# Kernel optimization log

Measured on AMD Instinct MI355X. Metric: run time of the kernel, lower is better.

## Reference

```python
import jax, jax.numpy as jnp
import numpy as np

B, S, T = 64, 128, 32
H, E, VOC = 512, 512, 32000
A = 2 * H  # atten_size


def setup_inputs() -> dict:
    key = jax.random.key(0)
    ks = jax.random.split(key, 10)
    n = lambda k, shp, sc: jax.random.normal(k, shp, jnp.float32) * sc
    return dict(
        encoder_output=n(ks[0], (B, S, A), 1.0),
        hs0=n(ks[1], (B, H), 1.0),
        cs0=n(ks[2], (B, H), 1.0),
        target=n(ks[3], (B, T, E), 1.0),
        wh_w=n(ks[4], (A, A), 0.02),          # Conv2d(2H, 2H, 1, bias=False) weight [out,in]
        ws_w=n(ks[5], (A, A), 0.02),          # Linear(2H, 2H)
        ws_b=jnp.zeros((A,), jnp.float32),
        we_w=n(ks[6], (A,), 0.02),            # Conv1d(2H, 1, 1, bias=False) weight [in]
        W_ih=n(ks[7], (4 * H, E), 0.02),      # LSTMCell params (torch gate order i,f,g,o)
        W_hh=n(ks[8], (4 * H, H), 0.02),
        b_ih=jnp.zeros((4 * H,), jnp.float32),
        b_hh=jnp.zeros((4 * H,), jnp.float32),
        Vp_w=n(ks[9], (VOC, 3 * H), 0.02),    # Linear(H + 2H, vocab)
        Vp_b=jnp.zeros((VOC,), jnp.float32),
    )


def reference(encoder_output, hs0, cs0, target, wh_w, ws_w, ws_b, we_w,
              W_ih, W_hh, b_ih, b_hh, Vp_w, Vp_b):
    # Faithful to torch: .view() is a raw row-major reshape, NOT a transpose.
    eo = encoder_output.reshape(B, A, S)                 # view(B, 2H, 1, S), squeeze the 1
    conv = jnp.einsum('oc,bcs->bos', wh_w, eo)           # 1x1 conv2d over channels
    enc_feat = conv.reshape(B, S, A)                     # view(B, -1, atten_size)

    def step(carry, x_t):
        hs, cs = carry
        df = jnp.concatenate([hs, cs], axis=1) @ ws_w.T + ws_b        # [B, A]
        comb = (enc_feat + df[:, None, :]).reshape(B, A, S)           # view(B, 2H, -1)
        e = jnp.einsum('c,bcs->bs', we_w, jnp.tanh(comb))             # conv1d(2H->1), squeeze
        a = jax.nn.softmax(e, axis=1)                                 # [B, S]
        h_star = jnp.einsum('bs,bsh->bh', a, encoder_output)          # bmm, squeeze
        # LSTMCell (torch gate order: i, f, g, o)
        gates = x_t @ W_ih.T + b_ih + hs @ W_hh.T + b_hh
        i, f, g, o = jnp.split(gates, 4, axis=1)
        cs_n = jax.nn.sigmoid(f) * cs + jax.nn.sigmoid(i) * jnp.tanh(g)
        hs_n = jax.nn.sigmoid(o) * jnp.tanh(cs_n)
        feat = jnp.concatenate([h_star, hs_n], axis=1)                # [B, 3H]
        out = jax.nn.log_softmax(feat @ Vp_w.T + Vp_b, axis=1)        # [B, vocab]
        return (hs_n, cs_n), out

    _, outs = jax.lax.scan(step, (hs0, cs0), jnp.swapaxes(target, 0, 1))
    return outs  # [T, B, vocab] (torch returns a list of T [B, vocab] arrays)
```

## Files before the change

### kernel.cpp

```cpp
#include <hip/hip_runtime.h>
#include <hip/hip_bf16.h>
#include <cstdint>
#include <cstddef>

typedef unsigned short u16;
typedef __attribute__((ext_vector_type(8))) short s16x8;
typedef __attribute__((ext_vector_type(4))) float f32x4;
typedef __attribute__((ext_vector_type(4))) unsigned short u16x4;

__device__ __forceinline__ float b2f(u16 u){ unsigned int i = ((unsigned int)u)<<16; float f; __builtin_memcpy(&f,&i,4); return f; }
__device__ __forceinline__ u16 f2b(float f){ unsigned int i; __builtin_memcpy(&i,&f,4); i = (i + 0x7fffu + ((i>>16)&1u))>>16; return (u16)i; }
__device__ __forceinline__ float tanh_f(float x){ return 1.f - 2.f/(1.f + __expf(2.f*x)); }
__device__ __forceinline__ float sig_f(float x){ return 1.f/(1.f + __expf(-x)); }

__device__ __forceinline__ void cp16(const u16* g, u16* l) {
  __builtin_amdgcn_global_load_lds((const __attribute__((address_space(1))) unsigned int*)g,
                                   (__attribute__((address_space(3))) unsigned int*)l, 16, 0, 0);
}

__global__ void k_cvt(const float* __restrict__ src, u16* __restrict__ dst, int n4) {
  int i = blockIdx.x*256 + threadIdx.x;
  if (i >= n4) return;
  float4 v = ((const float4*)src)[i];
  u16x4 o; o.x = f2b(v.x); o.y = f2b(v.y); o.z = f2b(v.z); o.w = f2b(v.w);
  ((u16x4*)dst)[i] = o;
}

__global__ __launch_bounds__(256, 2) void gemm_bt(
    const u16* __restrict__ A, const u16* __restrict__ B, void* __restrict__ Cv,
    const float* __restrict__ bias1, const float* __restrict__ bias2,
    int M, int N, int K, int ldA, int ldB, int ldC,
    long long strideA, long long strideB, long long strideC, int outBf16, int swz)
{
  __shared__ u16 As[128*32];
  __shared__ u16 Bs[128*32];
  const int bz = blockIdx.z;
  const u16* Ab = A + (size_t)bz*strideA;
  const u16* Bb = B + (size_t)bz*strideB;
  int bxx = blockIdx.x, byy = blockIdx.y;
  if (swz) {
    int nx = gridDim.x, ny = gridDim.y;
    int nwg = nx * ny;
    int orig = byy * nx + bxx;
    int cpx = nwg >> 3;
    int id = (orig & 7) * cpx + (orig >> 3);
    byy = id % ny;
    bxx = id / ny;
  }
  const int tn = bxx * 128;
  const int tm = byy * 128;
  const int tid = threadIdx.x, wid = tid>>6, lane = tid&63;
  const int wm = wid & 1, wn = wid >> 1;
  const int lrow = lane & 15, lk = (lane>>4)*8;

  f32x4 acc[4][4];
  #pragma unroll
  for (int i=0;i<4;++i)
    #pragma unroll
    for (int j=0;j<4;++j) acc[i][j] = (f32x4){0.f,0.f,0.f,0.f};

  const int srow = lane>>2;
  const int scol = (lane&3)*8;

  for (int k0 = 0; k0 < K; k0 += 32) {
    int c0 = wid, c1 = wid + 4;
    cp16(Ab + (size_t)(tm + c0*16 + srow)*ldA + k0 + scol, As + c0*512);
    cp16(Ab + (size_t)(tm + c1*16 + srow)*ldA + k0 + scol, As + c1*512);
    cp16(Bb + (size_t)(tn + c0*16 + srow)*ldB + k0 + scol, Bs + c0*512);
    cp16(Bb + (size_t)(tn + c1*16 + srow)*ldB + k0 + scol, Bs + c1*512);
    __syncthreads();

    s16x8 af[4], bfr[4];
    #pragma unroll
    for (int mt=0; mt<4; ++mt)
      af[mt] = *(const s16x8*)(As + (size_t)(wm*64 + mt*16 + lrow)*32 + lk);
    #pragma unroll
    for (int nt=0; nt<4; ++nt)
      bfr[nt] = *(const s16x8*)(Bs + (size_t)(wn*64 + nt*16 + lrow)*32 + lk);
    #pragma unroll
    for (int mt=0; mt<4; ++mt)
      #pragma unroll
      for (int nt=0; nt<4; ++nt)
        acc[mt][nt] = __builtin_amdgcn_mfma_f32_16x16x32_bf16(af[mt], bfr[nt], acc[mt][nt], 0,0,0);
    __syncthreads();
  }

  float* Cf = (float*)Cv + (size_t)bz*strideC;
  u16*   Ch = (u16*)Cv + (size_t)bz*strideC;
  #pragma unroll
  for (int mt=0; mt<4; ++mt) {
    #pragma unroll
    for (int nt=0; nt<4; ++nt) {
      int col = tn + wn*64 + nt*16 + (lane&15);
      float badd = 0.f;
      if (bias1) badd += bias1[col];
      if (bias2) badd += bias2[col];
      #pragma unroll
      for (int r=0; r<4; ++r) {
        int row = tm + wm*64 + mt*16 + (lane>>4)*4 + r;
        float v = acc[mt][nt][r] + badd;
        if (outBf16) Ch[(size_t)row*ldC + col] = f2b(v);
        else         Cf[(size_t)row*ldC + col] = v;
      }
    }
  }
}

__global__ __launch_bounds__(256, 2) void gemm_a16b32(
    const u16* __restrict__ A, const float* __restrict__ B, float* __restrict__ C,
    const float* __restrict__ bias, int M, int N, int K, int ldA, int ldB, int ldC, int swz)
{
  __shared__ u16 As[128*32];
  __shared__ u16 Bs[128*32];
  int bxx = blockIdx.x, byy = blockIdx.y;
  if (swz) {
    int nx = gridDim.x, ny = gridDim.y;
    int nwg = nx * ny;
    int orig = byy * nx + bxx;
    int cpx = nwg >> 3;
    int id = (orig & 7) * cpx + (orig >> 3);
    byy = id % ny;
    bxx = id / ny;
  }
  const int tn = bxx * 128;
  const int tm = byy * 128;
  const int tid = threadIdx.x, wid = tid>>6, lane = tid&63;
  const int wm = wid & 1, wn = wid >> 1;
  const int lrow = lane & 15, lk = (lane>>4)*8;

  f32x4 acc[4][4];
  #pragma unroll
  for (int i=0;i<4;++i)
    #pragma unroll
    for (int j=0;j<4;++j) acc[i][j] = (f32x4){0.f,0.f,0.f,0.f};

  const int srow = lane>>2;
  const int scol = (lane&3)*8;
  const int brow0 = tid>>3;
  const int bcol  = (tid&7)*4;

  for (int k0 = 0; k0 < K; k0 += 32) {
    int c0 = wid, c1 = wid + 4;
    cp16(A + (size_t)(tm + c0*16 + srow)*ldA + k0 + scol, As + c0*512);
    cp16(A + (size_t)(tm + c1*16 + srow)*ldA + k0 + scol, As + c1*512);
    #pragma unroll
    for (int rr=0; rr<4; ++rr) {
      int row = rr*32 + brow0;
      float4 v = *(const float4*)(B + (size_t)(tn + row)*ldB + k0 + bcol);
      u16x4 o; o.x = f2b(v.x); o.y = f2b(v.y); o.z = f2b(v.z); o.w = f2b(v.w);
      *(u16x4*)(Bs + (size_t)row*32 + bcol) = o;
    }
    __syncthreads();

    s16x8 af[4], bfr[4];
    #pragma unroll
    for (int mt=0; mt<4; ++mt)
      af[mt] = *(const s16x8*)(As + (size_t)(wm*64 + mt*16 + lrow)*32 + lk);
    #pragma unroll
    for (int nt=0; nt<4; ++nt)
      bfr[nt] = *(const s16x8*)(Bs + (size_t)(wn*64 + nt*16 + lrow)*32 + lk);
    #pragma unroll
    for (int mt=0; mt<4; ++mt)
      #pragma unroll
      for (int nt=0; nt<4; ++nt)
        acc[mt][nt] = __builtin_amdgcn_mfma_f32_16x16x32_bf16(af[mt], bfr[nt], acc[mt][nt], 0,0,0);
    __syncthreads();
  }

  #pragma unroll
  for (int mt=0; mt<4; ++mt) {
    #pragma unroll
    for (int nt=0; nt<4; ++nt) {
      int col = tn + wn*64 + nt*16 + (lane&15);
      float badd = bias ? bias[col] : 0.f;
      #pragma unroll
      for (int r=0; r<4; ++r) {
        int row = tm + wm*64 + mt*16 + (lane>>4)*4 + r;
        C[(size_t)row*ldC + col] = acc[mt][nt][r] + badd;
      }
    }
  }
}

__global__ void k_init(const float* __restrict__ hs0, const float* __restrict__ cs0,
                       u16* __restrict__ HSb0, u16* __restrict__ CSb0, float* __restrict__ CS0) {
  int i = blockIdx.x*256 + threadIdx.x;
  HSb0[i] = f2b(hs0[i]);
  float c = cs0[i];
  CSb0[i] = f2b(c);
  CS0[i] = c;
}

__global__ void k_x2(const float* __restrict__ target, u16* __restrict__ X2) {
  int r = blockIdx.x;
  int t = r >> 6, b = r & 63;
  float4 v = ((const float4*)(target + ((size_t)b*32 + t)*512))[threadIdx.x];
  u16x4 o; o.x = f2b(v.x); o.y = f2b(v.y); o.z = f2b(v.z); o.w = f2b(v.w);
  *(u16x4*)(X2 + (size_t)r*512 + threadIdx.x*4) = o;
}

__global__ void k_ebt(const float* __restrict__ enc, u16* __restrict__ EBt) {
  __shared__ u16 tile[64][72];
  int b = blockIdx.z;
  int c0 = blockIdx.x*64, s0 = blockIdx.y*64;
  int tid = threadIdx.x;
  int j = tid & 63, i0 = tid >> 6;
  const float* src = enc + (size_t)b*131072;
  for (int i = i0; i < 64; i += 4)
    tile[i][j] = f2b(src[(size_t)(c0+i)*128 + (s0+j)]);
  __syncthreads();
  u16* dst = EBt + (size_t)b*131072;
  for (int i = i0; i < 64; i += 4)
    dst[(size_t)(s0+i)*1024 + (c0+j)] = tile[j][i];
}

__global__ __launch_bounds__(256, 1) void lstm_step(
    const u16* __restrict__ HSb_t, const float* __restrict__ CS_t,
    const u16* __restrict__ Whh, const float* __restrict__ Xg_t,
    u16* __restrict__ HSb_n, float* __restrict__ CS_n, u16* __restrict__ CSb_n)
{
  int tid = threadIdx.x, wid = tid>>6, lane = tid&63;
  int hc = blockIdx.x * 16;
  int lr = lane & 15, lk = (lane>>4)*8;
  f32x4 acc[4];
  #pragma unroll
  for (int q=0;q<4;++q) acc[q] = (f32x4){0.f,0.f,0.f,0.f};
  int brow = wid*16 + lr;
  #pragma unroll
  for (int k0 = 0; k0 < 512; k0 += 32) {
    s16x8 a = *(const s16x8*)(HSb_t + (size_t)brow*512 + k0 + lk);
    #pragma unroll
    for (int q=0;q<4;++q) {
      int gj = q*512 + hc + lr;
      s16x8 bb = *(const s16x8*)(Whh + (size_t)gj*512 + k0 + lk);
      acc[q] = __builtin_amdgcn_mfma_f32_16x16x32_bf16(a, bb, acc[q], 0,0,0);
    }
  }
  int h = hc + lr;
  #pragma unroll
  for (int r=0;r<4;++r) {
    int b = wid*16 + (lane>>4)*4 + r;
    float gi = acc[0][r] + Xg_t[(size_t)b*2048 + h];
    float gf = acc[1][r] + Xg_t[(size_t)b*2048 + 512 + h];
    float gg = acc[2][r] + Xg_t[(size_t)b*2048 + 1024 + h];
    float go = acc[3][r] + Xg_t[(size_t)b*2048 + 1536 + h];
    float cs = CS_t[(size_t)b*512 + h];
    float csn = sig_f(gf)*cs + sig_f(gi)*tanh_f(gg);
    float hsn = sig_f(go)*tanh_f(csn);
    CS_n[(size_t)b*512 + h] = csn;
    HSb_n[(size_t)b*512 + h] = f2b(hsn);
    CSb_n[(size_t)b*512 + h] = f2b(csn);
  }
}

__global__ void k_dfa(const u16* __restrict__ HSb, const u16* __restrict__ CSb, u16* __restrict__ DfA) {
  int r = blockIdx.x; int t = r >> 6, b = r & 63;
  const uint2* hs = (const uint2*)(HSb + ((size_t)t*64 + b)*512);
  const uint2* cs = (const uint2*)(CSb + ((size_t)t*64 + b)*512);
  uint2* dst = (uint2*)(DfA + (size_t)r*1024);
  int tid = threadIdx.x;
  dst[tid] = (tid < 128) ? hs[tid] : cs[tid-128];
}

__global__ __launch_bounds__(256) void k_attn(
    const u16* __restrict__ G, const float* __restrict__ df,
    const float* __restrict__ we_w, const u16* __restrict__ Enc16,
    const u16* __restrict__ HSb, u16* __restrict__ Feat)
{
  int r = blockIdx.x, t = r>>6, b = r&63;
  int tid = threadIdx.x;
  __shared__ float weS[1024];
  __shared__ float eP[2][128];
  __shared__ float aS[128];
  __shared__ float redM, redS;
  for (int i=tid;i<1024;i+=256) weS[i] = we_w[i];
  __syncthreads();
  int s = tid & 127, cg = tid >> 7;
  const u16* Gb = G + (size_t)b*131072;
  const float* dfr = df + (size_t)r*1024;
  float p = 0.f;
  #pragma unroll 8
  for (int c = cg*512; c < cg*512 + 512; ++c) {
    float x = b2f(Gb[(size_t)c*128 + s]) + dfr[((c&7)<<7) + s];
    p += weS[c]*tanh_f(x);
  }
  eP[cg][s] = p;
  __syncthreads();
  if (tid < 128) aS[tid] = eP[0][tid] + eP[1][tid];
  __syncthreads();
  if (tid < 64) {
    float m = fmaxf(aS[tid], aS[tid+64]);
    #pragma unroll
    for (int off=32; off; off>>=1) m = fmaxf(m, __shfl_xor(m, off, 64));
    float sm = __expf(aS[tid]-m) + __expf(aS[tid+64]-m);
    #pragma unroll
    for (int off=32; off; off>>=1) sm += __shfl_xor(sm, off, 64);
    if (tid==0){ redM = m; redS = sm; }
  }
  __syncthreads();
  if (tid < 128) aS[tid] = __expf(aS[tid]-redM)/redS;
  __syncthreads();
  const u16* encb = Enc16 + (size_t)b*131072;
  u16* Fr = Feat + (size_t)r*1536;
  int h4 = tid*4;
  float a0=0,a1=0,a2=0,a3=0;
  for (int s2=0;s2<128;++s2) {
    float av = aS[s2];
    u16x4 v = *(const u16x4*)(encb + (size_t)s2*1024 + h4);
    a0 += av*b2f(v.x); a1 += av*b2f(v.y); a2 += av*b2f(v.z); a3 += av*b2f(v.w);
  }
  u16x4 o; o.x = f2b(a0); o.y = f2b(a1); o.z = f2b(a2); o.w = f2b(a3);
  *(u16x4*)(Fr + h4) = o;
  const u16* hsn = HSb + ((size_t)(t+1)*64 + b)*512;
  if (tid < 128) *(u16x4*)(Fr + 1024 + tid*4) = *(const u16x4*)(hsn + tid*4);
}

__global__ __launch_bounds__(256) void k_lsm(float* __restrict__ out) {
  int r = blockIdx.x;
  float* row = out + (size_t)r*32000;
  int tid = threadIdx.x, wid = tid>>6;
  __shared__ float redA[4], redB[4];
  float m = -3.0e38f;
  for (int i = tid*4; i < 32000; i += 1024) {
    float4 v = *(const float4*)(row + i);
    m = fmaxf(m, fmaxf(fmaxf(v.x, v.y), fmaxf(v.z, v.w)));
  }
  #pragma unroll
  for (int off=32; off; off>>=1) m = fmaxf(m, __shfl_xor(m, off, 64));
  if ((tid&63)==0) redA[wid] = m;
  __syncthreads();
  m = fmaxf(fmaxf(redA[0],redA[1]), fmaxf(redA[2],redA[3]));
  float sacc = 0.f;
  for (int i = tid*4; i < 32000; i += 1024) {
    float4 v = *(const float4*)(row + i);
    sacc += __expf(v.x-m) + __expf(v.y-m) + __expf(v.z-m) + __expf(v.w-m);
  }
  #pragma unroll
  for (int off=32; off; off>>=1) sacc += __shfl_xor(sacc, off, 64);
  if ((tid&63)==0) redB[wid] = sacc;
  __syncthreads();
  float lse = m + logf(redB[0]+redB[1]+redB[2]+redB[3]);
  for (int i = tid*4; i < 32000; i += 1024) {
    float4 v = *(const float4*)(row + i);
    v.x -= lse; v.y -= lse; v.z -= lse; v.w -= lse;
    *(float4*)(row + i) = v;
  }
}

extern "C" void kernel_launch(void* const* d_in, const int* in_sizes, int n_in,
                              void* d_out, int out_size, void* d_ws, size_t ws_size,
                              hipStream_t stream) {
  (void)in_sizes; (void)n_in; (void)out_size;
  const float* enc    = (const float*)d_in[0];
  const float* hs0    = (const float*)d_in[1];
  const float* cs0    = (const float*)d_in[2];
  const float* target = (const float*)d_in[3];
  const float* wh_w   = (const float*)d_in[4];
  const float* ws_w   = (const float*)d_in[5];
  const float* ws_b   = (const float*)d_in[6];
  const float* we_w   = (const float*)d_in[7];
  const float* W_ih   = (const float*)d_in[8];
  const float* W_hh   = (const float*)d_in[9];
  const float* b_ih   = (const float*)d_in[10];
  const float* b_hh   = (const float*)d_in[11];
  const float* Vp_w   = (const float*)d_in[12];
  const float* Vp_b   = (const float*)d_in[13];
  float* out = (float*)d_out;

  char* ws = (char*)d_ws;
  u16*   X2    = (u16*)  (ws + 0);
  u16*   EBt   = (u16*)  (ws + 2097152);
  u16*   G     = (u16*)  (ws + 18874368);
  float* Xg    = (float*)(ws + 35651584);
  u16*   Enc16 = (u16*)  (ws + 35651584);
  u16*   HSb   = (u16*)  (ws + 52428800);
  u16*   CSb   = (u16*)  (ws + 54591488);
  float* CS    = (float*)(ws + 56754176);
  u16*   DfA   = (u16*)  (ws + 61079552);
  float* dfb   = (float*)(ws + 65273856);
  u16*   Feat  = (u16*)  (ws + 73662464);
  u16*   Wih16 = (u16*)  (ws + 79953920);
  u16*   Whw16 = (u16*)  (ws + 82051072);
  u16*   Wsw16 = (u16*)  (ws + 84148224);
  u16*   Whh16 = (u16*)  (ws + 86245376);
  u16*   Vpw16 = (u16*)  (ws + 88342528);
  const bool tierA = ws_size >= (size_t)88342528 + 98304000;

  k_cvt<<<1024, 256, 0, stream>>>(W_ih, Wih16, 262144);
  k_cvt<<<1024, 256, 0, stream>>>(wh_w, Whw16, 262144);
  k_cvt<<<1024, 256, 0, stream>>>(ws_w, Wsw16, 262144);
  k_cvt<<<1024, 256, 0, stream>>>(W_hh, Whh16, 262144);
  if (tierA) k_cvt<<<48000, 256, 0, stream>>>(Vp_w, Vpw16, 12288000);

  k_init<<<128, 256, 0, stream>>>(hs0, cs0, HSb, CSb, CS);
  k_x2<<<2048, 128, 0, stream>>>(target, X2);
  k_ebt<<<dim3(16,2,64), 256, 0, stream>>>(enc, EBt);

  gemm_bt<<<dim3(16,16,1), 256, 0, stream>>>(X2, Wih16, Xg, b_ih, b_hh,
      2048, 2048, 512, 512, 512, 2048, 0, 0, 0, 0, 0);
  gemm_bt<<<dim3(1,8,64), 256, 0, stream>>>(Whw16, EBt, G, nullptr, nullptr,
      1024, 128, 1024, 1024, 1024, 128, 0, 131072, 131072, 1, 0);

  for (int t = 0; t < 32; ++t)
    lstm_step<<<32, 256, 0, stream>>>(HSb + (size_t)t*32768, CS + (size_t)t*32768, Whh16,
                                      Xg + (size_t)t*64*2048,
                                      HSb + (size_t)(t+1)*32768, CS + (size_t)(t+1)*32768,
                                      CSb + (size_t)(t+1)*32768);

  k_cvt<<<8192, 256, 0, stream>>>(enc, Enc16, 2097152);

  k_dfa<<<2048, 256, 0, stream>>>(HSb, CSb, DfA);
  gemm_bt<<<dim3(8,16,1), 256, 0, stream>>>(DfA, Wsw16, dfb, ws_b, nullptr,
      2048, 1024, 1024, 1024, 1024, 1024, 0, 0, 0, 0, 0);
  k_attn<<<2048, 256, 0, stream>>>(G, dfb, we_w, Enc16, HSb, Feat);

  if (tierA)
    gemm_bt<<<dim3(250,16,1), 256, 0, stream>>>(Feat, Vpw16, out, Vp_b, nullptr,
        2048, 32000, 1536, 1536, 1536, 32000, 0, 0, 0, 0, 1);
  else
    gemm_a16b32<<<dim3(250,16,1), 256, 0, stream>>>(Feat, Vp_w, out, Vp_b,
        2048, 32000, 1536, 1536, 1536, 32000, 1);

  k_lsm<<<2048, 256, 0, stream>>>(out);
}
```

Baseline: 1.501 ms.

## Add 256x256-tile 4-stage pipelined bf16 GEMM for vocab projection

Adds a new GEMM kernel with 256x256 output tiles, 512 threads, a 4-deep LDS ring fed by direct global-to-LDS copies, XOR-swizzled LDS layout, and split A/B staging interleaved with MFMA phases. It replaces the 128-tile GEMM for the large [2048x1536]x[1536x32000] vocab projection on the bf16 path. The goal is more operand reuse per LDS load and better overlap of memory with MFMA. In exchange it uses a large LDS footprint (128KB) and a big accumulator register file, which limits it to one workgroup per CU. Its 1000-block grid may also balance unevenly across CUs.

```diff
diff --git a/kernel.cpp b/kernel.cpp
--- a/kernel.cpp
+++ b/kernel.cpp
@@ -24,6 +24,128 @@
   float4 v = ((const float4*)src)[i];
   u16x4 o; o.x = f2b(v.x); o.y = f2b(v.y); o.z = f2b(v.z); o.w = f2b(v.w);
   ((u16x4*)dst)[i] = o;
+}
+
+__global__ __launch_bounds__(512, 1) void gemm256_bt(
+    const u16* __restrict__ A, const u16* __restrict__ B, float* __restrict__ C,
+    const float* __restrict__ bias, int M, int N, int K, int ldA, int ldB, int ldC)
+{
+  (void)M; (void)N;
+  __shared__ u16 As[4*8192];
+  __shared__ u16 Bs[4*8192];
+
+  {
+  }
+  const int nx = gridDim.x, ny = gridDim.y;
+  const int nwg = nx*ny;
+  const int orig = blockIdx.y*nx + blockIdx.x;
+  const int cpx = nwg >> 3;
+  const int id = (orig & 7)*cpx + (orig >> 3);
+  const int byy = id % ny;
+  const int bxx = id / ny;
+  const int tn = bxx*256, tm = byy*256;
+
+  const int tid = threadIdx.x, wid = tid>>6, lane = tid&63;
+  const int wm = wid & 1, wn = wid >> 1;
+  const int lr = lane & 15, ks = lane >> 4;
+  const int NT = K >> 5;
+
+  f32x4 acc[8][4];
+  #pragma unroll
+  for (int m=0;m<8;++m)
+    #pragma unroll
+    for (int n=0;n<4;++n) acc[m][n] = (f32x4){0.f,0.f,0.f,0.f};
+
+  const int st_r0 = wid*16 + (lane>>2);
+  const int st_sl0 = (lane&3) ^ ((st_r0>>1)&3);
+  const int st_r1 = 128 + st_r0;
+  const int st_sl1 = (lane&3) ^ ((st_r1>>1)&3);
+
+  #define STAGE_A(kt_) do { \
+    u16* dst = As + (((kt_)&3)<<13) + (wid<<9); \
+    cp16(A + (size_t)(tm + st_r0)*ldA + (kt_)*32 + st_sl0*8, dst); \
+    cp16(A + (size_t)(tm + st_r1)*ldA + (kt_)*32 + st_sl1*8, dst + 4096); \
+  } while(0)
+  #define STAGE_B(kt_) do { \
+    u16* dst = Bs + (((kt_)&3)<<13) + (wid<<9); \
+    cp16(B + (size_t)(tn + st_r0)*ldB + (kt_)*32 + st_sl0*8, dst); \
+    cp16(B + (size_t)(tn + st_r1)*ldB + (kt_)*32 + st_sl1*8, dst + 4096); \
+  } while(0)
+
+  {
+    int pmax = NT < 3 ? NT : 3;
+    for (int j=0;j<pmax;++j) { STAGE_A(j); STAGE_B(j); }
+  }
+  asm volatile("s_waitcnt vmcnt(8)" ::: "memory");
+  __builtin_amdgcn_s_barrier();
+
+  for (int kt = 0; kt < NT; ++kt) {
+    const u16* Ap = As + ((kt&3)<<13);
+    const u16* Bp = Bs + ((kt&3)<<13);
+    const bool st = (kt + 3) < NT;
+
+    s16x8 bf[4], af[4];
+    #pragma unroll
+    for (int n=0;n<4;++n) {
+      int rb = wn*64 + n*16 + lr;
+      bf[n] = *(const s16x8*)(Bp + rb*32 + ((ks ^ ((rb>>1)&3))<<3));
+    }
+    #pragma unroll
+    for (int m=0;m<4;++m) {
+      int ra = wm*128 + m*16 + lr;
+      af[m] = *(const s16x8*)(Ap + ra*32 + ((ks ^ ((ra>>1)&3))<<3));
+    }
+    if (st) STAGE_A(kt+3);
+    __builtin_amdgcn_s_barrier();
+    __builtin_amdgcn_s_setprio(1);
+    #pragma unroll
+    for (int m=0;m<4;++m)
+      #pragma unroll
+      for (int n=0;n<4;++n)
+        acc[m][n] = __builtin_amdgcn_mfma_f32_16x16x32_bf16(af[m], bf[n], acc[m][n], 0,0,0);
+    __builtin_amdgcn_s_setprio(0);
+    __builtin_amdgcn_s_barrier();
+
+    s16x8 ag[4];
+    #pragma unroll
+    for (int m=0;m<4;++m) {
+      int ra = wm*128 + (m+4)*16 + lr;
+      ag[m] = *(const s16x8*)(Ap + ra*32 + ((ks ^ ((ra>>1)&3))<<3));
+    }
+    if (st) STAGE_B(kt+3);
+    __builtin_amdgcn_s_barrier();
+    __builtin_amdgcn_s_setprio(1);
+    #pragma unroll
+    for (int m=0;m<4;++m)
+      #pragma unroll
+      for (int n=0;n<4;++n)
+        acc[m+4][n] = __builtin_amdgcn_mfma_f32_16x16x32_bf16(ag[m], bf[n], acc[m+4][n], 0,0,0);
+    __builtin_amdgcn_s_setprio(0);
+    {
+      int lastStaged = (kt+3 < NT) ? (kt+3) : (NT-1);
+      int cnt = lastStaged - kt;
+      if (cnt == 3)      asm volatile("s_waitcnt vmcnt(8)" ::: "memory");
+      else if (cnt == 2) asm volatile("s_waitcnt vmcnt(4)" ::: "memory");
+      else if (cnt == 1) asm volatile("s_waitcnt vmcnt(0)" ::: "memory");
+    }
+    __builtin_amdgcn_s_barrier();
+  }
+  #undef STAGE_A
+  #undef STAGE_B
+
+  #pragma unroll
+  for (int m=0;m<8;++m) {
+    #pragma unroll
+    for (int n=0;n<4;++n) {
+      int col = tn + wn*64 + n*16 + lr;
+      float badd = bias ? bias[col] : 0.f;
+      #pragma unroll
+      for (int r=0;r<4;++r) {
+        int row = tm + wm*128 + m*16 + ks*4 + r;
+        C[(size_t)row*ldC + col] = acc[m][n][r] + badd;
+      }
+    }
+  }
 }
 
 __global__ __launch_bounds__(256, 2) void gemm_bt(
@@ -415,8 +537,8 @@
   k_attn<<<2048, 256, 0, stream>>>(G, dfb, we_w, Enc16, HSb, Feat);
 
   if (tierA)
-    gemm_bt<<<dim3(250,16,1), 256, 0, stream>>>(Feat, Vpw16, out, Vp_b, nullptr,
-        2048, 32000, 1536, 1536, 1536, 32000, 0, 0, 0, 0, 1);
+    gemm256_bt<<<dim3(125, 8, 1), 512, 0, stream>>>(Feat, Vpw16, out, Vp_b,
+        2048, 32000, 1536, 1536, 1536, 32000);
   else
     gemm_a16b32<<<dim3(250,16,1), 256, 0, stream>>>(Feat, Vp_w, out, Vp_b,
         2048, 32000, 1536, 1536, 1536, 32000, 1);
```

Result: faster. 1.469 ms (-2.1%).

## Add 256x256-tile four-stage pipelined GEMM for vocab projection

Applied to the files above, without the earlier changes.

Adds a new 512-thread bf16 MFMA GEMM with 256x256 output tiles, a four-buffer async global-to-LDS pipeline, XOR-swizzled LDS layout, interleaved load/compute phases with priority hints, and an XCD-aware block remap. It replaces the 128x128 gemm_bt for the large 2048x32000x1536 projection on the tierA path. The aim is to raise arithmetic intensity and hide memory latency in the dominant GEMM. The cost is one block per CU, high register use for 32 accumulators, and 32000 only tiling into 125 column blocks, which makes the tail less balanced.

```diff
diff --git a/kernel.cpp b/kernel.cpp
--- a/kernel.cpp
+++ b/kernel.cpp
@@ -24,6 +24,135 @@
   float4 v = ((const float4*)src)[i];
   u16x4 o; o.x = f2b(v.x); o.y = f2b(v.y); o.z = f2b(v.z); o.w = f2b(v.w);
   ((u16x4*)dst)[i] = o;
+}
+
+__global__ __launch_bounds__(512, 1) void gemm256_bt(
+    const u16* __restrict__ A, const u16* __restrict__ B, float* __restrict__ C,
+    const float* __restrict__ bias, int M, int N, int K, int ldA, int ldB, int ldC)
+{
+  (void)M; (void)N;
+  __shared__ u16 As[4*8192];
+  __shared__ u16 Bs[4*8192];
+
+  const int nx = gridDim.x, ny = gridDim.y;
+  const int nwg = nx*ny;
+  const int orig = blockIdx.y*nx + blockIdx.x;
+  const int cpx = nwg >> 3;
+  const int id = (orig & 7)*cpx + (orig >> 3);
+  const int byy = id % ny;
+  const int bxx = id / ny;
+  const int tn = bxx*256, tm = byy*256;
+
+  const int tid = threadIdx.x, wid = tid>>6, lane = tid&63;
+  const int wm = wid & 1, wn = wid >> 1;
+  const int lr = lane & 15, ks = lane >> 4;
+  const int NT = K >> 5;
+
+  f32x4 acc[8][4];
+  #pragma unroll
+  for (int m=0;m<8;++m)
+    #pragma unroll
+    for (int n=0;n<4;++n) acc[m][n] = (f32x4){0.f,0.f,0.f,0.f};
+
+  const int st_r0 = wid*16 + (lane>>2);
+  const int st_sl0 = (lane&3) ^ ((st_r0>>1)&3);
+  const int st_r1 = 128 + st_r0;
+  const int st_sl1 = (lane&3) ^ ((st_r1>>1)&3);
+
+  #define STAGE_A(kt_, wb_) do { \
+    u16* dst = As + ((wb_)*8192) + (wid<<9); \
+    cp16(A + (size_t)(tm + st_r0)*ldA + (kt_)*32 + st_sl0*8, dst); \
+    cp16(A + (size_t)(tm + st_r1)*ldA + (kt_)*32 + st_sl1*8, dst + 4096); \
+  } while(0)
+  #define STAGE_B(kt_, wb_) do { \
+    u16* dst = Bs + ((wb_)*8192) + (wid<<9); \
+    cp16(B + (size_t)(tn + st_r0)*ldB + (kt_)*32 + st_sl0*8, dst); \
+    cp16(B + (size_t)(tn + st_r1)*ldB + (kt_)*32 + st_sl1*8, dst + 4096); \
+  } while(0)
+
+  STAGE_A(0, 0); STAGE_B(0, 0);
+  STAGE_A(1, 1); STAGE_B(1, 1);
+  STAGE_A(2, 2); STAGE_B(2, 2);
+  asm volatile("s_waitcnt vmcnt(8)" ::: "memory");
+  __builtin_amdgcn_s_barrier();
+
+  #define PHASE_PAIR(u_, rb_, wb_) do { \
+    const int kt = kb + (u_); \
+    const u16* Ap = As + (rb_)*8192; \
+    const u16* Bp = Bs + (rb_)*8192; \
+    const bool st = (kt + 3) < NT; \
+     \
+    s16x8 bf[4], af[4]; \
+    _Pragma("unroll") \
+    for (int n=0;n<4;++n) { \
+      int rb = wn*64 + n*16 + lr; \
+      bf[n] = *(const s16x8*)(Bp + rb*32 + ((ks ^ ((rb>>1)&3))<<3)); \
+    } \
+    _Pragma("unroll") \
+    for (int m=0;m<4;++m) { \
+      int ra = wm*128 + m*16 + lr; \
+      af[m] = *(const s16x8*)(Ap + ra*32 + ((ks ^ ((ra>>1)&3))<<3)); \
+    } \
+    if (st) STAGE_A(kt+3, wb_); \
+    __builtin_amdgcn_s_barrier(); \
+    __builtin_amdgcn_s_setprio(1); \
+    _Pragma("unroll") \
+    for (int m=0;m<4;++m) \
+      _Pragma("unroll") \
+      for (int n=0;n<4;++n) \
+        acc[m][n] = __builtin_amdgcn_mfma_f32_16x16x32_bf16(af[m], bf[n], acc[m][n], 0,0,0); \
+    __builtin_amdgcn_s_setprio(0); \
+    __builtin_amdgcn_s_barrier(); \
+     \
+    s16x8 ag[4]; \
+    _Pragma("unroll") \
+    for (int m=0;m<4;++m) { \
+      int ra = wm*128 + (m+4)*16 + lr; \
+      ag[m] = *(const s16x8*)(Ap + ra*32 + ((ks ^ ((ra>>1)&3))<<3)); \
+    } \
+    if (st) STAGE_B(kt+3, wb_); \
+    __builtin_amdgcn_s_barrier(); \
+    __builtin_amdgcn_s_setprio(1); \
+    _Pragma("unroll") \
+    for (int m=0;m<4;++m) \
+      _Pragma("unroll") \
+      for (int n=0;n<4;++n) \
+        acc[m+4][n] = __builtin_amdgcn_mfma_f32_16x16x32_bf16(ag[m], bf[n], acc[m+4][n], 0,0,0); \
+    __builtin_amdgcn_s_setprio(0); \
+     \
+    { \
+      int lastStaged = (kt+3 < NT) ? (kt+3) : (NT-1); \
+      int cnt = lastStaged - kt; \
+      if (cnt == 3)      asm volatile("s_waitcnt vmcnt(8)" ::: "memory"); \
+      else if (cnt == 2) asm volatile("s_waitcnt vmcnt(4)" ::: "memory"); \
+      else if (cnt == 1) asm volatile("s_waitcnt vmcnt(0)" ::: "memory"); \
+    } \
+    __builtin_amdgcn_s_barrier(); \
+  } while(0)
+
+  for (int kb = 0; kb < NT; kb += 4) {
+    PHASE_PAIR(0, 0, 3);
+    PHASE_PAIR(1, 1, 0);
+    PHASE_PAIR(2, 2, 1);
+    PHASE_PAIR(3, 3, 2);
+  }
+  #undef PHASE_PAIR
+  #undef STAGE_A
+  #undef STAGE_B
+
+  #pragma unroll
+  for (int m=0;m<8;++m) {
+    #pragma unroll
+    for (int n=0;n<4;++n) {
+      int col = tn + wn*64 + n*16 + lr;
+      float badd = bias ? bias[col] : 0.f;
+      #pragma unroll
+      for (int r=0;r<4;++r) {
+        int row = tm + wm*128 + m*16 + ks*4 + r;
+        C[(size_t)row*ldC + col] = acc[m][n][r] + badd;
+      }
+    }
+  }
 }
 
 __global__ __launch_bounds__(256, 2) void gemm_bt(
@@ -415,8 +544,8 @@
   k_attn<<<2048, 256, 0, stream>>>(G, dfb, we_w, Enc16, HSb, Feat);
 
   if (tierA)
-    gemm_bt<<<dim3(250,16,1), 256, 0, stream>>>(Feat, Vpw16, out, Vp_b, nullptr,
-        2048, 32000, 1536, 1536, 1536, 32000, 0, 0, 0, 0, 1);
+    gemm256_bt<<<dim3(125, 8, 1), 512, 0, stream>>>(Feat, Vpw16, out, Vp_b,
+        2048, 32000, 1536, 1536, 1536, 32000);
   else
     gemm_a16b32<<<dim3(250,16,1), 256, 0, stream>>>(Feat, Vp_w, out, Vp_b,
         2048, 32000, 1536, 1536, 1536, 32000, 1);
```

Result: faster. 1.469 ms (-2.1%).
